# Kernel tuning notes

Measured on AMD Instinct MI355X. Metric: run time of the kernel, lower is better.

Reference implementation:

```python
import jax, jax.numpy as jnp
import numpy as np

N_NODES = 50000
D = 128
E_RAND = 640000
ALPHA = 0.2  # LeakyReLU negative slope


def setup_inputs() -> dict:
    key = jax.random.key(0)
    k1, k2, k3, k4, k5 = jax.random.split(key, 5)
    inputs = jax.random.normal(k1, (N_NODES, D), dtype=jnp.float32) * 0.1
    # xavier_normal with gain=1.414 as in the torch module
    W = jax.random.normal(k2, (D, D), dtype=jnp.float32) * (1.414 * np.sqrt(2.0 / (D + D)))
    a = jax.random.normal(k3, (2 * D,), dtype=jnp.float32) * (1.414 * np.sqrt(2.0 / (1 + 2 * D)))
    # random edges + self-loops so every node has at least one outgoing edge (nonzero rowsum)
    src = jnp.concatenate([jax.random.randint(k4, (E_RAND,), 0, N_NODES), jnp.arange(N_NODES)])
    dst = jnp.concatenate([jax.random.randint(k5, (E_RAND,), 0, N_NODES), jnp.arange(N_NODES)])
    edge = jnp.stack([src, dst]).astype(jnp.int64)
    return {"inputs": inputs, "edge": edge, "W": W, "a": a}


def reference(inputs, edge, W, a):
    N = inputs.shape[0]
    src, dst = edge[0], edge[1]
    h = inputs @ W  # [N, D]
    # a @ [h_src; h_dst] per edge == h_src @ a[:D] + h_dst @ a[D:]
    score = h[src] @ a[:D] + h[dst] @ a[D:]  # [E]
    edge_e = jnp.exp(jax.nn.leaky_relu(score, negative_slope=ALPHA))  # [E]
    # sparse.mm(coo(edge, edge_e), ones): rowsum over src (coalesce sums duplicates)
    e_rowsum = jax.ops.segment_sum(edge_e, src, num_segments=N)  # [N]
    # sparse.mm(coo(edge, edge_e), h): weighted aggregation of h[dst] into src rows
    h_prime = jax.ops.segment_sum(edge_e[:, None] * h[dst], src, num_segments=N)  # [N, D]
    h_prime = h_prime / e_rowsum[:, None]
    return jax.nn.elu(h_prime)
```

## Files before the change

### kernel.cpp

```cpp
#include <hip/hip_runtime.h>
#include <hip/hip_bf16.h>


constexpr int D    = 128;
constexpr int CH   = 16384;
constexpr int CAPB = 1280;

typedef __attribute__((ext_vector_type(8))) short bf16x8;
typedef __attribute__((ext_vector_type(4))) float f32x4;

__device__ __forceinline__ short f2bf(float f) {
    unsigned u = __float_as_uint(f);
    unsigned r = (u + 0x7fffu + ((u >> 16) & 1u)) >> 16;
    return (short)r;
}
__device__ __forceinline__ float bf2f(short b) {
    return __uint_as_float(((unsigned)(unsigned short)b) << 16);
}
__device__ __forceinline__ short2 pk_bf16(float x, float y) {
    __hip_bfloat162 bb = __float22bfloat162_rn(make_float2(x, y));
    short2 r;
    __builtin_memcpy(&r, &bb, 4);
    return r;
}

__global__ __launch_bounds__(512) void bin_and_gemm(
    const float* __restrict__ X, const float* __restrict__ W,
    const float* __restrict__ a,
    const int* __restrict__ src, const int* __restrict__ dst,
    int* __restrict__ desc, int* __restrict__ binned,
    short* __restrict__ h, float* __restrict__ s1, float* __restrict__ s2,
    int NB, int NC, int N, int E) {
    __shared__ int sbuf[CH];
    __shared__ int hist[784];
    __shared__ int sarr[1024];
    if (blockIdx.x < (unsigned)NC) {
        const int c = blockIdx.x, t = threadIdx.x;
        for (int u = t; u < NB; u += 512) hist[u] = 0;
        __syncthreads();
        const int lo = c * CH, hi = min(lo + CH, E);
        const int len = hi - lo;
        const int hi4 = lo + (len & ~3);
        for (int i = lo + t * 4; i < hi4; i += 2048) {
            const int4 s4 = *(const int4*)(src + i);
            atomicAdd(&hist[s4.x >> 6], 1);
            atomicAdd(&hist[s4.y >> 6], 1);
            atomicAdd(&hist[s4.z >> 6], 1);
            atomicAdd(&hist[s4.w >> 6], 1);
        }
        for (int i = hi4 + t; i < hi; i += 512)
            atomicAdd(&hist[src[i] >> 6], 1);
        __syncthreads();
        for (int u = t; u < 1024; u += 512) sarr[u] = (u < NB) ? hist[u] : 0;
        __syncthreads();
        for (int o = 1; o < 1024; o <<= 1) {
            int v[2];
#pragma unroll
            for (int k = 0; k < 2; ++k) {
                const int idx = t + k * 512;
                v[k] = (idx >= o) ? sarr[idx - o] : 0;
            }
            __syncthreads();
#pragma unroll
            for (int k = 0; k < 2; ++k) sarr[t + k * 512] += v[k];
            __syncthreads();
        }
        for (int u = t; u < NB; u += 512) {
            const int ex = sarr[u] - hist[u];
            desc[(size_t)c * NB + u] = ex | (hist[u] << 15);
            sarr[u] = ex;
            hist[u] = 0;
        }
        __syncthreads();
        for (int i = lo + t * 4; i < hi4; i += 2048) {
            const int4 s4 = *(const int4*)(src + i);
            const int4 d4 = *(const int4*)(dst + i);
            const int sv[4] = {s4.x, s4.y, s4.z, s4.w};
            const int dv[4] = {d4.x, d4.y, d4.z, d4.w};
#pragma unroll
            for (int j = 0; j < 4; ++j) {
                const int b = sv[j] >> 6;
                const int r = atomicAdd(&hist[b], 1);
                sbuf[sarr[b] + r] = ((sv[j] & 63) << 16) | dv[j];
            }
        }
        for (int i = hi4 + t; i < hi; i += 512) {
            const int s = src[i];
            const int b = s >> 6;
            const int r = atomicAdd(&hist[b], 1);
            sbuf[sarr[b] + r] = ((s & 63) << 16) | dst[i];
        }
        __syncthreads();
        const int len4 = len & ~3;
        for (int i = t * 4; i < len4; i += 2048)
            *(int4*)(binned + (size_t)c * CH + i) = *(const int4*)(sbuf + i);
        for (int i = len4 + t; i < len; i += 512)
            binned[(size_t)c * CH + i] = sbuf[i];
        return;
    }
    short* lbw = (short*)sbuf;
    for (int f4 = threadIdx.x; f4 < 4096; f4 += 512) {
        const float4 w4 = *(const float4*)(W + f4 * 4);
        const float wv[4] = {w4.x, w4.y, w4.z, w4.w};
        const int f0 = f4 * 4;
#pragma unroll
        for (int u = 0; u < 4; ++u) {
            const int f = f0 + u;
            const int k = f >> 7, n = f & 127;
            const int sl = ((k >> 5) * 8 + (n >> 4)) * 64 +
                           ((k >> 3) & 3) * 16 + (n & 15);
            lbw[sl * 8 + (k & 7)] = f2bf(wv[u]);
        }
    }
    __syncthreads();
    const int wave = threadIdx.x >> 6, lane = threadIdx.x & 63;
    const int r0 = (blockIdx.x - NC) * 128 + wave * 16;
    const int m = lane & 15, q = lane >> 4;
    const int arow = r0 + m;
    const bool rowok = arow < N;
    const float* xp = X + (size_t)arow * D + q * 8;

    f32x4 acc[8] = {};
#pragma unroll
    for (int s = 0; s < 4; ++s) {
        float4 xa = {0, 0, 0, 0}, xb = {0, 0, 0, 0};
        if (rowok) {
            xa = *(const float4*)(xp + s * 32);
            xb = *(const float4*)(xp + s * 32 + 4);
        }
        bf16x8 af;
        short2 c0 = pk_bf16(xa.x, xa.y), c1 = pk_bf16(xa.z, xa.w);
        short2 c2 = pk_bf16(xb.x, xb.y), c3 = pk_bf16(xb.z, xb.w);
        af[0] = c0.x; af[1] = c0.y; af[2] = c1.x; af[3] = c1.y;
        af[4] = c2.x; af[5] = c2.y; af[6] = c3.x; af[7] = c3.y;
#pragma unroll
        for (int t = 0; t < 8; ++t) {
            bf16x8 bf = *(const bf16x8*)(lbw + ((s * 8 + t) * 64 + lane) * 8);
            acc[t] = __builtin_amdgcn_mfma_f32_16x16x32_bf16(af, bf, acc[t], 0, 0, 0);
        }
    }
    float a1v[8], a2v[8];
#pragma unroll
    for (int t = 0; t < 8; ++t) {
        a1v[t] = a[t * 16 + m];
        a2v[t] = a[D + t * 16 + m];
    }
    float p1[4] = {0, 0, 0, 0}, p2[4] = {0, 0, 0, 0};
#pragma unroll
    for (int t = 0; t < 8; ++t) {
        short2 h01 = pk_bf16(acc[t][0], acc[t][1]);
        short2 h23 = pk_bf16(acc[t][2], acc[t][3]);
        const short hb[4] = {h01.x, h01.y, h23.x, h23.y};
#pragma unroll
        for (int i = 0; i < 4; ++i) {
            const int row = r0 + q * 4 + i;
            if (row < N) h[(size_t)row * D + t * 16 + m] = hb[i];
            const float hr = bf2f(hb[i]);
            p1[i] += hr * a1v[t];
            p2[i] += hr * a2v[t];
        }
    }
#pragma unroll
    for (int off = 1; off < 16; off <<= 1) {
#pragma unroll
        for (int i = 0; i < 4; ++i) {
            p1[i] += __shfl_xor(p1[i], off);
            p2[i] += __shfl_xor(p2[i], off);
        }
    }
    if (m < 4) {
        const int row = r0 + q * 4 + m;
        if (row < N) {
            const float v1 = (m == 0) ? p1[0] : (m == 1) ? p1[1] : (m == 2) ? p1[2] : p1[3];
            const float v2 = (m == 0) ? p2[0] : (m == 1) ? p2[1] : (m == 2) ? p2[2] : p2[3];
            s1[row] = v1;
            s2[row] = v2;
        }
    }
}

__global__ __launch_bounds__(512) void aggregate(
    const int* __restrict__ binned, const int* __restrict__ desc,
    const float* __restrict__ s1, const float* __restrict__ s2,
    const short* __restrict__ h, float* __restrict__ out,
    int NB, int NC, int N) {
    __shared__ int elist[CAPB];
    __shared__ unsigned short dlist[CAPB + 16];
    __shared__ int rdesc[64], sc[64];
    __shared__ int ncnt[64], exclp[64], pcnt[64];
    __shared__ float ss1[64];
    const int b = blockIdx.x, tid = threadIdx.x;
    const int n0 = b * 64;
    if (tid < 64) {
        ncnt[tid] = 0;
        pcnt[tid] = 0;
        ss1[tid] = (n0 + tid < N) ? s1[n0 + tid] : 0.f;
        const int dsc = (tid < NC) ? desc[(size_t)tid * NB + b] : 0;
        rdesc[tid] = dsc;
        int v = dsc >> 15;
#pragma unroll
        for (int o = 1; o < 64; o <<= 1) {
            const int u = __shfl_up(v, o);
            if (tid >= o) v += u;
        }
        sc[tid] = v;
    }
    __syncthreads();
    const int total = sc[63];
    const int nE = min(total, CAPB);
    {
        const int gid = tid >> 4, l16 = tid & 15;
        for (int c = gid; c < NC; c += 32) {
            const int dsc = rdesc[c];
            const int off = dsc & 0x7FFF;
            const int cnt = dsc >> 15;
            const int p0 = sc[c] - cnt;
            for (int j = l16; j < cnt; j += 16) {
                const int p = p0 + j;
                if (p < CAPB) elist[p] = binned[(size_t)c * CH + off + j];
            }
        }
    }
    __syncthreads();
    for (int i = tid; i < nE; i += 512) atomicAdd(&ncnt[elist[i] >> 16], 1);
    __syncthreads();
    if (tid < 64) {
        int v = ncnt[tid];
#pragma unroll
        for (int o = 1; o < 64; o <<= 1) {
            const int u = __shfl_up(v, o);
            if (tid >= o) v += u;
        }
        exclp[tid] = v - ncnt[tid];
    }
    __syncthreads();
    const int tot2 = exclp[63] + ncnt[63];
    if (tid < 16) dlist[tot2 + tid] = 0;
    for (int i = tid; i < nE; i += 512) {
        const int e = elist[i];
        const int r = e >> 16;
        const int k = atomicAdd(&pcnt[r], 1);
        dlist[exclp[r] + k] = (unsigned short)(e & 0xFFFF);
    }
    __syncthreads();

    const int wid = tid >> 6, lane = tid & 63;
    const int g = lane >> 4, m = lane & 15;
    const int m8 = m * 8;
#pragma unroll 1
    for (int t = 0; t < 8; ++t) {
        const int r = wid * 8 + t;
        const int n = n0 + r;
        if (n >= N) continue;
        const int cnt = ncnt[r];
        if (cnt == 0) continue;
        const int beg = exclp[r];
        const float s1n = ss1[r];

        float acc[8] = {};
        float rs = 0.f;
#pragma unroll 1
        for (int k0 = 0; k0 < cnt; k0 += 16) {
            const int dA = dlist[beg + k0 + g];
            const int dB = dlist[beg + k0 + 4 + g];
            const int dC = dlist[beg + k0 + 8 + g];
            const int dD = dlist[beg + k0 + 12 + g];
            const float sA = s2[dA], sB = s2[dB], sC = s2[dC], sD = s2[dD];
            const bf16x8 rA = *(const bf16x8*)(h + (dA << 7) + m8);
            const bf16x8 rB = *(const bf16x8*)(h + (dB << 7) + m8);
            const bf16x8 rC = *(const bf16x8*)(h + (dC << 7) + m8);
            const bf16x8 rD = *(const bf16x8*)(h + (dD << 7) + m8);

            float xA = s1n + sA; xA = xA > 0.f ? xA : 0.2f * xA;
            float eA = __expf(xA);
            if (k0 + g >= cnt) eA = 0.f;
            float xB = s1n + sB; xB = xB > 0.f ? xB : 0.2f * xB;
            float eB = __expf(xB);
            if (k0 + 4 + g >= cnt) eB = 0.f;
            float xC = s1n + sC; xC = xC > 0.f ? xC : 0.2f * xC;
            float eC = __expf(xC);
            if (k0 + 8 + g >= cnt) eC = 0.f;
            float xD = s1n + sD; xD = xD > 0.f ? xD : 0.2f * xD;
            float eD = __expf(xD);
            if (k0 + 12 + g >= cnt) eD = 0.f;
#pragma unroll
            for (int j = 0; j < 8; ++j)
                acc[j] += eA * bf2f(rA[j]) + eB * bf2f(rB[j]) +
                          eC * bf2f(rC[j]) + eD * bf2f(rD[j]);
            rs += (eA + eB) + (eC + eD);
        }
#pragma unroll
        for (int off = 16; off <= 32; off <<= 1) {
            rs += __shfl_xor(rs, off);
#pragma unroll
            for (int j = 0; j < 8; ++j) acc[j] += __shfl_xor(acc[j], off);
        }
        if (g == 0) {
            const float inv = 1.f / rs;
            float o[8];
#pragma unroll
            for (int j = 0; j < 8; ++j) {
                const float v = acc[j] * inv;
                o[j] = v > 0.f ? v : __expf(v) - 1.f;
            }
            float* op = out + (size_t)n * D + m8;
            *(float4*)op       = make_float4(o[0], o[1], o[2], o[3]);
            *(float4*)(op + 4) = make_float4(o[4], o[5], o[6], o[7]);
        }
    }
}

extern "C" void kernel_launch(void* const* d_in, const int* in_sizes, int n_in,
                              void* d_out, int out_size, void* d_ws, size_t ws_size,
                              hipStream_t stream) {
    const float* X    = (const float*)d_in[0];
    const int*   edge = (const int*)d_in[1];
    const float* W    = (const float*)d_in[2];
    const float* a    = (const float*)d_in[3];
    float* out = (float*)d_out;

    const int N = in_sizes[0] / D;
    const int E = in_sizes[1] / 2;
    const int* src = edge;
    const int* dst = edge + E;

    const int NB = (N + 63) / 64;
    const int NC = (E + CH - 1) / CH;
    const int NG = (N + 127) / 128;

    char* ws = (char*)d_ws;
    short* h    = (short*)ws; ws += (size_t)N * D * sizeof(short);
    int* binned = (int*)ws;   ws += (size_t)NC * CH * sizeof(int);
    int* desc   = (int*)ws;   ws += (size_t)NC * NB * sizeof(int);
    float* s1   = (float*)ws; ws += (size_t)N * sizeof(float);
    float* s2   = (float*)ws; ws += (size_t)N * sizeof(float);

    bin_and_gemm<<<NC + NG, 512, 0, stream>>>(X, W, a, src, dst, desc, binned,
                                              h, s1, s2, NB, NC, N, E);
    aggregate<<<NB, 512, 0, stream>>>(binned, desc, s1, s2, h, out, NB, NC, N);
}
```

Measured before the change: 137.2 us.

## Fuse binning, GEMM and aggregation into one persistent kernel with global barriers

Merges the two kernels into a single persistent kernel launched with 512 blocks. Binning and GEMM blocks signal completion through global atomic counters, and every block then runs a grid-stride aggregation loop, waiting on those counters first. The aggregation builds its edge lists before it waits for the GEMM, so that setup overlaps with the tail of the GEMM. This removes a kernel launch boundary and the idle tail between stages, but it adds spin-wait barriers that deadlock unless all 512 blocks are co-resident, plus a memset launch to reset the counters.

```diff
diff --git a/kernel.cpp b/kernel.cpp
--- a/kernel.cpp
+++ b/kernel.cpp
@@ -24,18 +24,21 @@
     return r;
 }
 
-__global__ __launch_bounds__(512) void bin_and_gemm(
+__global__ __launch_bounds__(512, 4) void gat_fused(
     const float* __restrict__ X, const float* __restrict__ W,
     const float* __restrict__ a,
     const int* __restrict__ src, const int* __restrict__ dst,
     int* __restrict__ desc, int* __restrict__ binned,
     short* __restrict__ h, float* __restrict__ s1, float* __restrict__ s2,
-    int NB, int NC, int N, int E) {
+    float* __restrict__ out, int* __restrict__ bar,
+    int NB, int NC, int NG, int N, int E) {
     __shared__ int sbuf[CH];
     __shared__ int hist[784];
     __shared__ int sarr[1024];
-    if (blockIdx.x < (unsigned)NC) {
-        const int c = blockIdx.x, t = threadIdx.x;
+    const int bid = blockIdx.x, tid = threadIdx.x;
+
+    if (bid < NC) {
+        const int c = bid, t = tid;
         for (int u = t; u < NB; u += 512) hist[u] = 0;
         __syncthreads();
         const int lo = c * CH, hi = min(lo + CH, E);
@@ -96,216 +99,243 @@
             *(int4*)(binned + (size_t)c * CH + i) = *(const int4*)(sbuf + i);
         for (int i = len4 + t; i < len; i += 512)
             binned[(size_t)c * CH + i] = sbuf[i];
-        return;
+        __syncthreads();
+        if (tid == 0)
+            __hip_atomic_fetch_add(&bar[0], 1, __ATOMIC_RELEASE,
+                                   __HIP_MEMORY_SCOPE_AGENT);
+    } else if (bid < NC + NG) {
+        short* lbw = (short*)sbuf;
+        for (int f4 = tid; f4 < 4096; f4 += 512) {
+            const float4 w4 = *(const float4*)(W + f4 * 4);
+            const float wv[4] = {w4.x, w4.y, w4.z, w4.w};
+            const int f0 = f4 * 4;
+#pragma unroll
+            for (int u = 0; u < 4; ++u) {
+                const int f = f0 + u;
+                const int k = f >> 7, n = f & 127;
+                const int sl = ((k >> 5) * 8 + (n >> 4)) * 64 +
+                               ((k >> 3) & 3) * 16 + (n & 15);
+                lbw[sl * 8 + (k & 7)] = f2bf(wv[u]);
+            }
+        }
+        __syncthreads();
+        const int wave = tid >> 6, lane = tid & 63;
+        const int r0 = (bid - NC) * 128 + wave * 16;
+        const int m = lane & 15, q = lane >> 4;
+        const int arow = r0 + m;
+        const bool rowok = arow < N;
+        const float* xp = X + (size_t)arow * D + q * 8;
+
+        f32x4 acc[8] = {};
+#pragma unroll
+        for (int s = 0; s < 4; ++s) {
+            float4 xa = {0, 0, 0, 0}, xb = {0, 0, 0, 0};
+            if (rowok) {
+                xa = *(const float4*)(xp + s * 32);
+                xb = *(const float4*)(xp + s * 32 + 4);
+            }
+            bf16x8 af;
+            short2 c0 = pk_bf16(xa.x, xa.y), c1 = pk_bf16(xa.z, xa.w);
+            short2 c2 = pk_bf16(xb.x, xb.y), c3 = pk_bf16(xb.z, xb.w);
+            af[0] = c0.x; af[1] = c0.y; af[2] = c1.x; af[3] = c1.y;
+            af[4] = c2.x; af[5] = c2.y; af[6] = c3.x; af[7] = c3.y;
+#pragma unroll
+            for (int t = 0; t < 8; ++t) {
+                bf16x8 bf = *(const bf16x8*)(lbw + ((s * 8 + t) * 64 + lane) * 8);
+                acc[t] = __builtin_amdgcn_mfma_f32_16x16x32_bf16(af, bf, acc[t], 0, 0, 0);
+            }
+        }
+        float a1v[8], a2v[8];
+#pragma unroll
+        for (int t = 0; t < 8; ++t) {
+            a1v[t] = a[t * 16 + m];
+            a2v[t] = a[D + t * 16 + m];
+        }
+        float p1[4] = {0, 0, 0, 0}, p2[4] = {0, 0, 0, 0};
+#pragma unroll
+        for (int t = 0; t < 8; ++t) {
+            short2 h01 = pk_bf16(acc[t][0], acc[t][1]);
+            short2 h23 = pk_bf16(acc[t][2], acc[t][3]);
+            const short hb[4] = {h01.x, h01.y, h23.x, h23.y};
+#pragma unroll
+            for (int i = 0; i < 4; ++i) {
+                const int row = r0 + q * 4 + i;
+                if (row < N) h[(size_t)row * D + t * 16 + m] = hb[i];
+                const float hr = bf2f(hb[i]);
+                p1[i] += hr * a1v[t];
+                p2[i] += hr * a2v[t];
+            }
+        }
+#pragma unroll
+        for (int off = 1; off < 16; off <<= 1) {
+#pragma unroll
+            for (int i = 0; i < 4; ++i) {
+                p1[i] += __shfl_xor(p1[i], off);
+                p2[i] += __shfl_xor(p2[i], off);
+            }
+        }
+        if (m < 4) {
+            const int row = r0 + q * 4 + m;
+            if (row < N) {
+                const float v1 = (m == 0) ? p1[0] : (m == 1) ? p1[1] : (m == 2) ? p1[2] : p1[3];
+                const float v2 = (m == 0) ? p2[0] : (m == 1) ? p2[1] : (m == 2) ? p2[2] : p2[3];
+                s1[row] = v1;
+                s2[row] = v2;
+            }
+        }
+        __syncthreads();
+        if (tid == 0)
+            __hip_atomic_fetch_add(&bar[1], 1, __ATOMIC_RELEASE,
+                                   __HIP_MEMORY_SCOPE_AGENT);
     }
-    short* lbw = (short*)sbuf;
-    for (int f4 = threadIdx.x; f4 < 4096; f4 += 512) {
-        const float4 w4 = *(const float4*)(W + f4 * 4);
-        const float wv[4] = {w4.x, w4.y, w4.z, w4.w};
-        const int f0 = f4 * 4;
-#pragma unroll
-        for (int u = 0; u < 4; ++u) {
-            const int f = f0 + u;
-            const int k = f >> 7, n = f & 127;
-            const int sl = ((k >> 5) * 8 + (n >> 4)) * 64 +
-                           ((k >> 3) & 3) * 16 + (n & 15);
-            lbw[sl * 8 + (k & 7)] = f2bf(wv[u]);
-        }
+
+    if (tid == 0) {
+        while (__hip_atomic_load(&bar[0], __ATOMIC_ACQUIRE,
+                                 __HIP_MEMORY_SCOPE_AGENT) < NC)
+            __builtin_amdgcn_s_sleep(16);
     }
     __syncthreads();
-    const int wave = threadIdx.x >> 6, lane = threadIdx.x & 63;
-    const int r0 = (blockIdx.x - NC) * 128 + wave * 16;
-    const int m = lane & 15, q = lane >> 4;
-    const int arow = r0 + m;
-    const bool rowok = arow < N;
-    const float* xp = X + (size_t)arow * D + q * 8;
-
-    f32x4 acc[8] = {};
-#pragma unroll
-    for (int s = 0; s < 4; ++s) {
-        float4 xa = {0, 0, 0, 0}, xb = {0, 0, 0, 0};
-        if (rowok) {
-            xa = *(const float4*)(xp + s * 32);
-            xb = *(const float4*)(xp + s * 32 + 4);
-        }
-        bf16x8 af;
-        short2 c0 = pk_bf16(xa.x, xa.y), c1 = pk_bf16(xa.z, xa.w);
-        short2 c2 = pk_bf16(xb.x, xb.y), c3 = pk_bf16(xb.z, xb.w);
-        af[0] = c0.x; af[1] = c0.y; af[2] = c1.x; af[3] = c1.y;
-        af[4] = c2.x; af[5] = c2.y; af[6] = c3.x; af[7] = c3.y;
-#pragma unroll
+
+    int* elist = sbuf;
+    unsigned short* dlist = (unsigned short*)(sbuf + CAPB);
+    int* rdesc = hist;
+    int* scn   = hist + 128;
+    int* ncnt  = sarr;
+    int* exclp = sarr + 64;
+    int* pcnt  = sarr + 128;
+    float* ss1 = (float*)(sarr + 192);
+
+    bool gemm_ready = false;
+    for (int b = bid; b < NB; b += gridDim.x) {
+        __syncthreads();
+        const int n0 = b * 64;
+        if (tid < 64) {
+            ncnt[tid] = 0;
+            pcnt[tid] = 0;
+            const int dsc = (tid < NC) ? desc[(size_t)tid * NB + b] : 0;
+            rdesc[tid] = dsc;
+            int v = dsc >> 15;
+#pragma unroll
+            for (int o = 1; o < 64; o <<= 1) {
+                const int u = __shfl_up(v, o);
+                if (tid >= o) v += u;
+            }
+            scn[tid] = v;
+        }
+        __syncthreads();
+        const int total = scn[63];
+        const int nE = min(total, CAPB);
+        {
+            const int gid = tid >> 4, l16 = tid & 15;
+            for (int c = gid; c < NC; c += 32) {
+                const int dsc = rdesc[c];
+                const int off = dsc & 0x7FFF;
+                const int cnt = dsc >> 15;
+                const int p0 = scn[c] - cnt;
+                for (int j = l16; j < cnt; j += 16) {
+                    const int p = p0 + j;
+                    if (p < CAPB) elist[p] = binned[(size_t)c * CH + off + j];
+                }
+            }
+        }
+        __syncthreads();
+        for (int i = tid; i < nE; i += 512) atomicAdd(&ncnt[elist[i] >> 16], 1);
+        __syncthreads();
+        if (tid < 64) {
+            int v = ncnt[tid];
+#pragma unroll
+            for (int o = 1; o < 64; o <<= 1) {
+                const int u = __shfl_up(v, o);
+                if (tid >= o) v += u;
+            }
+            exclp[tid] = v - ncnt[tid];
+        }
+        __syncthreads();
+        const int tot2 = exclp[63] + ncnt[63];
+        if (tid < 16) dlist[tot2 + tid] = 0;
+        for (int i = tid; i < nE; i += 512) {
+            const int e = elist[i];
+            const int r = e >> 16;
+            const int k = atomicAdd(&pcnt[r], 1);
+            dlist[exclp[r] + k] = (unsigned short)(e & 0xFFFF);
+        }
+        __syncthreads();
+
+        if (!gemm_ready) {
+            if (tid == 0) {
+                while (__hip_atomic_load(&bar[1], __ATOMIC_ACQUIRE,
+                                         __HIP_MEMORY_SCOPE_AGENT) < NG)
+                    __builtin_amdgcn_s_sleep(16);
+            }
+            __syncthreads();
+            gemm_ready = true;
+        }
+        if (tid < 64) ss1[tid] = (n0 + tid < N) ? s1[n0 + tid] : 0.f;
+        __syncthreads();
+
+        const int wid = tid >> 6, lane = tid & 63;
+        const int g = lane >> 4, m = lane & 15;
+        const int m8 = m * 8;
+#pragma unroll 1
         for (int t = 0; t < 8; ++t) {
-            bf16x8 bf = *(const bf16x8*)(lbw + ((s * 8 + t) * 64 + lane) * 8);
-            acc[t] = __builtin_amdgcn_mfma_f32_16x16x32_bf16(af, bf, acc[t], 0, 0, 0);
-        }
-    }
-    float a1v[8], a2v[8];
-#pragma unroll
-    for (int t = 0; t < 8; ++t) {
-        a1v[t] = a[t * 16 + m];
-        a2v[t] = a[D + t * 16 + m];
-    }
-    float p1[4] = {0, 0, 0, 0}, p2[4] = {0, 0, 0, 0};
-#pragma unroll
-    for (int t = 0; t < 8; ++t) {
-        short2 h01 = pk_bf16(acc[t][0], acc[t][1]);
-        short2 h23 = pk_bf16(acc[t][2], acc[t][3]);
-        const short hb[4] = {h01.x, h01.y, h23.x, h23.y};
-#pragma unroll
-        for (int i = 0; i < 4; ++i) {
-            const int row = r0 + q * 4 + i;
-            if (row < N) h[(size_t)row * D + t * 16 + m] = hb[i];
-            const float hr = bf2f(hb[i]);
-            p1[i] += hr * a1v[t];
-            p2[i] += hr * a2v[t];
-        }
-    }
-#pragma unroll
-    for (int off = 1; off < 16; off <<= 1) {
-#pragma unroll
-        for (int i = 0; i < 4; ++i) {
-            p1[i] += __shfl_xor(p1[i], off);
-            p2[i] += __shfl_xor(p2[i], off);
-        }
-    }
-    if (m < 4) {
-        const int row = r0 + q * 4 + m;
-        if (row < N) {
-            const float v1 = (m == 0) ? p1[0] : (m == 1) ? p1[1] : (m == 2) ? p1[2] : p1[3];
-            const float v2 = (m == 0) ? p2[0] : (m == 1) ? p2[1] : (m == 2) ? p2[2] : p2[3];
-            s1[row] = v1;
-            s2[row] = v2;
-        }
-    }
-}
-
-__global__ __launch_bounds__(512) void aggregate(
-    const int* __restrict__ binned, const int* __restrict__ desc,
-    const float* __restrict__ s1, const float* __restrict__ s2,
-    const short* __restrict__ h, float* __restrict__ out,
-    int NB, int NC, int N) {
-    __shared__ int elist[CAPB];
-    __shared__ unsigned short dlist[CAPB + 16];
-    __shared__ int rdesc[64], sc[64];
-    __shared__ int ncnt[64], exclp[64], pcnt[64];
-    __shared__ float ss1[64];
-    const int b = blockIdx.x, tid = threadIdx.x;
-    const int n0 = b * 64;
-    if (tid < 64) {
-        ncnt[tid] = 0;
-        pcnt[tid] = 0;
-        ss1[tid] = (n0 + tid < N) ? s1[n0 + tid] : 0.f;
-        const int dsc = (tid < NC) ? desc[(size_t)tid * NB + b] : 0;
-        rdesc[tid] = dsc;
-        int v = dsc >> 15;
-#pragma unroll
-        for (int o = 1; o < 64; o <<= 1) {
-            const int u = __shfl_up(v, o);
-            if (tid >= o) v += u;
-        }
-        sc[tid] = v;
-    }
-    __syncthreads();
-    const int total = sc[63];
-    const int nE = min(total, CAPB);
-    {
-        const int gid = tid >> 4, l16 = tid & 15;
-        for (int c = gid; c < NC; c += 32) {
-            const int dsc = rdesc[c];
-            const int off = dsc & 0x7FFF;
-            const int cnt = dsc >> 15;
-            const int p0 = sc[c] - cnt;
-            for (int j = l16; j < cnt; j += 16) {
-                const int p = p0 + j;
-                if (p < CAPB) elist[p] = binned[(size_t)c * CH + off + j];
-            }
-        }
-    }
-    __syncthreads();
-    for (int i = tid; i < nE; i += 512) atomicAdd(&ncnt[elist[i] >> 16], 1);
-    __syncthreads();
-    if (tid < 64) {
-        int v = ncnt[tid];
-#pragma unroll
-        for (int o = 1; o < 64; o <<= 1) {
-            const int u = __shfl_up(v, o);
-            if (tid >= o) v += u;
-        }
-        exclp[tid] = v - ncnt[tid];
-    }
-    __syncthreads();
-    const int tot2 = exclp[63] + ncnt[63];
-    if (tid < 16) dlist[tot2 + tid] = 0;
-    for (int i = tid; i < nE; i += 512) {
-        const int e = elist[i];
-        const int r = e >> 16;
-        const int k = atomicAdd(&pcnt[r], 1);
-        dlist[exclp[r] + k] = (unsigned short)(e & 0xFFFF);
-    }
-    __syncthreads();
-
-    const int wid = tid >> 6, lane = tid & 63;
-    const int g = lane >> 4, m = lane & 15;
-    const int m8 = m * 8;
+            const int r = wid * 8 + t;
+            const int n = n0 + r;
+            if (n >= N) continue;
+            const int cnt = ncnt[r];
+            if (cnt == 0) continue;
+            const int beg = exclp[r];
+            const float s1n = ss1[r];
+
+            float acc[8] = {};
+            float rs = 0.f;
 #pragma unroll 1
-    for (int t = 0; t < 8; ++t) {
-        const int r = wid * 8 + t;
-        const int n = n0 + r;
-        if (n >= N) continue;
-        const int cnt = ncnt[r];
-        if (cnt == 0) continue;
-        const int beg = exclp[r];
-        const float s1n = ss1[r];
-
-        float acc[8] = {};
-        float rs = 0.f;
-#pragma unroll 1
-        for (int k0 = 0; k0 < cnt; k0 += 16) {
-            const int dA = dlist[beg + k0 + g];
-            const int dB = dlist[beg + k0 + 4 + g];
-            const int dC = dlist[beg + k0 + 8 + g];
-            const int dD = dlist[beg + k0 + 12 + g];
-            const float sA = s2[dA], sB = s2[dB], sC = s2[dC], sD = s2[dD];
-            const bf16x8 rA = *(const bf16x8*)(h + (dA << 7) + m8);
-            const bf16x8 rB = *(const bf16x8*)(h + (dB << 7) + m8);
-            const bf16x8 rC = *(const bf16x8*)(h + (dC << 7) + m8);
-            const bf16x8 rD = *(const bf16x8*)(h + (dD << 7) + m8);
-
-            float xA = s1n + sA; xA = xA > 0.f ? xA : 0.2f * xA;
-            float eA = __expf(xA);
-            if (k0 + g >= cnt) eA = 0.f;
-            float xB = s1n + sB; xB = xB > 0.f ? xB : 0.2f * xB;
-            float eB = __expf(xB);
-            if (k0 + 4 + g >= cnt) eB = 0.f;
-            float xC = s1n + sC; xC = xC > 0.f ? xC : 0.2f * xC;
-            float eC = __expf(xC);
-            if (k0 + 8 + g >= cnt) eC = 0.f;
-            float xD = s1n + sD; xD = xD > 0.f ? xD : 0.2f * xD;
-            float eD = __expf(xD);
-            if (k0 + 12 + g >= cnt) eD = 0.f;
-#pragma unroll
-            for (int j = 0; j < 8; ++j)
-                acc[j] += eA * bf2f(rA[j]) + eB * bf2f(rB[j]) +
-                          eC * bf2f(rC[j]) + eD * bf2f(rD[j]);
-            rs += (eA + eB) + (eC + eD);
-        }
-#pragma unroll
-        for (int off = 16; off <= 32; off <<= 1) {
-            rs += __shfl_xor(rs, off);
-#pragma unroll
-            for (int j = 0; j < 8; ++j) acc[j] += __shfl_xor(acc[j], off);
-        }
-        if (g == 0) {
-            const float inv = 1.f / rs;
-            float o[8];
-#pragma unroll
-            for (int j = 0; j < 8; ++j) {
-                const float v = acc[j] * inv;
-                o[j] = v > 0.f ? v : __expf(v) - 1.f;
-            }
-            float* op = out + (size_t)n * D + m8;
-            *(float4*)op       = make_float4(o[0], o[1], o[2], o[3]);
-            *(float4*)(op + 4) = make_float4(o[4], o[5], o[6], o[7]);
+            for (int k0 = 0; k0 < cnt; k0 += 16) {
+                const int dA = dlist[beg + k0 + g];
+                const int dB = dlist[beg + k0 + 4 + g];
+                const int dC = dlist[beg + k0 + 8 + g];
+                const int dD = dlist[beg + k0 + 12 + g];
+                const float sA = s2[dA], sB = s2[dB], sC = s2[dC], sD = s2[dD];
+                const bf16x8 rA = *(const bf16x8*)(h + (dA << 7) + m8);
+                const bf16x8 rB = *(const bf16x8*)(h + (dB << 7) + m8);
+                const bf16x8 rC = *(const bf16x8*)(h + (dC << 7) + m8);
+                const bf16x8 rD = *(const bf16x8*)(h + (dD << 7) + m8);
+
+                float xA = s1n + sA; xA = xA > 0.f ? xA : 0.2f * xA;
+                float eA = __expf(xA);
+                if (k0 + g >= cnt) eA = 0.f;
+                float xB = s1n + sB; xB = xB > 0.f ? xB : 0.2f * xB;
+                float eB = __expf(xB);
+                if (k0 + 4 + g >= cnt) eB = 0.f;
+                float xC = s1n + sC; xC = xC > 0.f ? xC : 0.2f * xC;
+                float eC = __expf(xC);
+                if (k0 + 8 + g >= cnt) eC = 0.f;
+                float xD = s1n + sD; xD = xD > 0.f ? xD : 0.2f * xD;
+                float eD = __expf(xD);
+                if (k0 + 12 + g >= cnt) eD = 0.f;
+#pragma unroll
+                for (int j = 0; j < 8; ++j)
+                    acc[j] += eA * bf2f(rA[j]) + eB * bf2f(rB[j]) +
+                              eC * bf2f(rC[j]) + eD * bf2f(rD[j]);
+                rs += (eA + eB) + (eC + eD);
+            }
+#pragma unroll
+            for (int off = 16; off <= 32; off <<= 1) {
+                rs += __shfl_xor(rs, off);
+#pragma unroll
+                for (int j = 0; j < 8; ++j) acc[j] += __shfl_xor(acc[j], off);
+            }
+            if (g == 0) {
+                const float inv = 1.f / rs;
+                float o[8];
+#pragma unroll
+                for (int j = 0; j < 8; ++j) {
+                    const float v = acc[j] * inv;
+                    o[j] = v > 0.f ? v : __expf(v) - 1.f;
+                }
+                float* op = out + (size_t)n * D + m8;
+                *(float4*)op       = make_float4(o[0], o[1], o[2], o[3]);
+                *(float4*)(op + 4) = make_float4(o[4], o[5], o[6], o[7]);
+            }
         }
     }
 }
@@ -319,14 +349,14 @@
     const float* a    = (const float*)d_in[3];
     float* out = (float*)d_out;
 
-    const int N = in_sizes[0] / D;
-    const int E = in_sizes[1] / 2;
+    int N = in_sizes[0] / D;
+    int E = in_sizes[1] / 2;
     const int* src = edge;
     const int* dst = edge + E;
 
-    const int NB = (N + 63) / 64;
-    const int NC = (E + CH - 1) / CH;
-    const int NG = (N + 127) / 128;
+    int NB = (N + 63) / 64;
+    int NC = (E + CH - 1) / CH;
+    int NG = (N + 127) / 128;
 
     char* ws = (char*)d_ws;
     short* h    = (short*)ws; ws += (size_t)N * D * sizeof(short);
@@ -334,8 +364,10 @@
     int* desc   = (int*)ws;   ws += (size_t)NC * NB * sizeof(int);
     float* s1   = (float*)ws; ws += (size_t)N * sizeof(float);
     float* s2   = (float*)ws; ws += (size_t)N * sizeof(float);
-
-    bin_and_gemm<<<NC + NG, 512, 0, stream>>>(X, W, a, src, dst, desc, binned,
-                                              h, s1, s2, NB, NC, N, E);
-    aggregate<<<NB, 512, 0, stream>>>(binned, desc, s1, s2, h, out, NB, NC, N);
-}
+    int* bar    = (int*)ws;   ws += 4 * sizeof(int);
+
+    hipMemsetAsync(bar, 0, 2 * sizeof(int), stream);
+    gat_fused<<<512, 512, 0, stream>>>(X, W, a, src, dst, desc, binned,
+                                       h, s1, s2, out, bar,
+                                       NB, NC, NG, N, E);
+}
```

Result: slower. 203.6 us (+48.4%).
